# Kernel optimization log

Measured on AMD Instinct MI355X. Metric: run time of the kernel, lower is better.

The kernel has to match this reference:

```python
import jax, jax.numpy as jnp
import numpy as np

D = 512  # feature_dim


def setup_inputs() -> dict:
    key = jax.random.key(0)
    ks = jax.random.split(key, 10)
    s = 1.0 / np.sqrt(D)
    s2 = 1.0 / np.sqrt(2 * D)
    return {
        "X": jax.random.normal(ks[0], (8, 2048, D), dtype=jnp.float32),
        "Y": jax.random.normal(ks[1], (8, 2048, D), dtype=jnp.float32),
        "W_xq": jax.random.uniform(ks[2], (D, D), jnp.float32, -s, s),
        "b_xq": jax.random.uniform(ks[3], (D,), jnp.float32, -s, s),
        "W_yq": jax.random.uniform(ks[4], (D, D), jnp.float32, -s, s),
        "b_yq": jax.random.uniform(ks[5], (D,), jnp.float32, -s, s),
        "W_fk": jax.random.uniform(ks[6], (D, 2 * D), jnp.float32, -s2, s2),
        "b_fk": jax.random.uniform(ks[7], (D,), jnp.float32, -s2, s2),
        "W_fv": jax.random.uniform(ks[8], (D, 2 * D), jnp.float32, -s2, s2),
        "b_fv": jax.random.uniform(ks[9], (D,), jnp.float32, -s2, s2),
    }


def reference(X, Y, W_xq, b_xq, W_yq, b_yq, W_fk, b_fk, W_fv, b_fv):
    # Dropout is evaluated in eval mode (identity).
    scale = 1.0 / jnp.sqrt(jnp.asarray(D, X.dtype))
    Q1 = jnp.einsum('bsd,ed->bse', X, W_xq) + b_xq  # [B,S,D]
    Q2 = jnp.einsum('bsd,ed->bse', Y, W_yq) + b_yq
    Q_cat = jnp.concatenate([Q1, Q2], axis=-1)      # [B,S,2D]
    K_f = jnp.einsum('bsc,ec->bse', Q_cat, W_fk) + b_fk
    V_f = jnp.einsum('bsc,ec->bse', Q_cat, W_fv) + b_fv

    def attend(Q):
        scores = jnp.einsum('bqd,bkd->bqk', Q, K_f) * scale  # [B,S,S]
        A = jax.nn.softmax(scores, axis=-1)
        return jnp.einsum('bqk,bkd->bqd', A, V_f)

    U_A1 = X + attend(Q1)
    U_A2 = Y + attend(Q2)
    return U_A1 + U_A2
```

## Files before the change

### kernel.cpp

```cpp
#include <hip/hip_runtime.h>


#define B_    8
#define S_    2048
#define D_    512
#define M_TOT (B_ * S_)

typedef __bf16 bf16_t;
typedef __bf16 bf16x8 __attribute__((ext_vector_type(8)));
typedef __bf16 bf16x4 __attribute__((ext_vector_type(4)));
typedef float  f32x4  __attribute__((ext_vector_type(4)));

typedef __attribute__((address_space(1))) const void* gas_cv;
typedef __attribute__((address_space(3))) void*       las_v;

__device__ __forceinline__ f32x4 mfma16(bf16x8 a, bf16x8 b, f32x4 c) {
    return __builtin_amdgcn_mfma_f32_16x16x32_bf16(a, b, c, 0, 0, 0);
}
__device__ __forceinline__ void load_lds16(const void* g, void* l) {
    __builtin_amdgcn_global_load_lds((gas_cv)g, (las_v)l, 16, 0, 0);
}

__global__ __launch_bounds__(256) void k_qgemm(
    const float* __restrict__ X, const float* __restrict__ Y,
    const float* __restrict__ Wxq, const float* __restrict__ bxq,
    const float* __restrict__ Wyq, const float* __restrict__ byq,
    bf16_t* __restrict__ Qcat)
{
    __shared__ __attribute__((aligned(16))) bf16_t Al[128 * 40];
    __shared__ __attribute__((aligned(16))) bf16_t Bl[128 * 40];
    const int m0 = blockIdx.x * 128;
    const int n0 = blockIdx.y * 128;
    const bool second = (n0 >= 512);
    const float* A    = second ? Y : X;
    const float* W    = second ? Wyq : Wxq;
    const float* bias = second ? byq : bxq;
    const int nw = n0 & 511;
    const int t    = threadIdx.x;
    const int lane = t & 63;
    const int wv   = t >> 6;
    const int wm   = (wv & 1) * 64;
    const int wn   = (wv >> 1) * 64;
    const int l15  = lane & 15;
    const int quad = lane >> 4;

    f32x4 acc[4][4] = {};

    for (int k0 = 0; k0 < 512; k0 += 32) {
        __syncthreads();
#pragma unroll
        for (int p = 0; p < 4; ++p) {
            const int lin = p * 256 + t;
            const int row = lin >> 3;
            const int ch  = (lin & 7) * 4;
            const float4 va = *(const float4*)(A + (size_t)(m0 + row) * 512 + k0 + ch);
            bf16x4 pa = { (bf16_t)va.x, (bf16_t)va.y, (bf16_t)va.z, (bf16_t)va.w };
            *(bf16x4*)(Al + row * 40 + ch) = pa;
            const float4 vb = *(const float4*)(W + (size_t)(nw + row) * 512 + k0 + ch);
            bf16x4 pb = { (bf16_t)vb.x, (bf16_t)vb.y, (bf16_t)vb.z, (bf16_t)vb.w };
            *(bf16x4*)(Bl + row * 40 + ch) = pb;
        }
        __syncthreads();
        bf16x8 af[4], bfr[4];
#pragma unroll
        for (int i = 0; i < 4; ++i)
            af[i] = *(const bf16x8*)(Al + (wm + i * 16 + l15) * 40 + quad * 8);
#pragma unroll
        for (int i = 0; i < 4; ++i)
            bfr[i] = *(const bf16x8*)(Bl + (wn + i * 16 + l15) * 40 + quad * 8);
#pragma unroll
        for (int mt = 0; mt < 4; ++mt)
#pragma unroll
            for (int nt = 0; nt < 4; ++nt)
                acc[mt][nt] = mfma16(af[mt], bfr[nt], acc[mt][nt]);
    }

#pragma unroll
    for (int nt = 0; nt < 4; ++nt) {
        const int col  = n0 + wn + nt * 16 + l15;
        const float bv = bias[col & 511];
#pragma unroll
        for (int mt = 0; mt < 4; ++mt) {
            const int rowb = m0 + wm + mt * 16 + quad * 4;
#pragma unroll
            for (int r = 0; r < 4; ++r)
                Qcat[(size_t)(rowb + r) * 1024 + col] = (bf16_t)(acc[mt][nt][r] + bv);
        }
    }
}

__global__ __launch_bounds__(256) void k_kvgemm(
    const bf16_t* __restrict__ Qcat,
    const float* __restrict__ Wfk, const float* __restrict__ bfk,
    const float* __restrict__ Wfv, const float* __restrict__ bfv,
    bf16_t* __restrict__ Kf, bf16_t* __restrict__ Vt)
{
    __shared__ __attribute__((aligned(16))) union {
        struct { bf16_t Al[128 * 40]; bf16_t Bl[128 * 40]; } g;
        bf16_t T[128 * 132];
    } sm;
    const int m0 = blockIdx.x * 128;
    const int n0 = blockIdx.y * 128;
    const bool isV = (n0 >= 512);
    const float* W    = isV ? Wfv : Wfk;
    const float* bias = isV ? bfv : bfk;
    const int nw = n0 & 511;
    const int t    = threadIdx.x;
    const int lane = t & 63;
    const int wv   = t >> 6;
    const int wm   = (wv & 1) * 64;
    const int wn   = (wv >> 1) * 64;
    const int l15  = lane & 15;
    const int quad = lane >> 4;

    f32x4 acc[4][4] = {};

    for (int k0 = 0; k0 < 1024; k0 += 32) {
        __syncthreads();
#pragma unroll
        for (int p = 0; p < 2; ++p) {
            const int lin = p * 256 + t;
            const int row = lin >> 2;
            const int ch  = (lin & 3) * 8;
            *(bf16x8*)(sm.g.Al + row * 40 + ch) =
                *(const bf16x8*)(Qcat + (size_t)(m0 + row) * 1024 + k0 + ch);
        }
#pragma unroll
        for (int p = 0; p < 4; ++p) {
            const int lin = p * 256 + t;
            const int row = lin >> 3;
            const int ch  = (lin & 7) * 4;
            const float4 vb = *(const float4*)(W + (size_t)(nw + row) * 1024 + k0 + ch);
            bf16x4 pb = { (bf16_t)vb.x, (bf16_t)vb.y, (bf16_t)vb.z, (bf16_t)vb.w };
            *(bf16x4*)(sm.g.Bl + row * 40 + ch) = pb;
        }
        __syncthreads();
        bf16x8 af[4], bfr[4];
#pragma unroll
        for (int i = 0; i < 4; ++i)
            af[i] = *(const bf16x8*)(sm.g.Al + (wm + i * 16 + l15) * 40 + quad * 8);
#pragma unroll
        for (int i = 0; i < 4; ++i)
            bfr[i] = *(const bf16x8*)(sm.g.Bl + (wn + i * 16 + l15) * 40 + quad * 8);
#pragma unroll
        for (int mt = 0; mt < 4; ++mt)
#pragma unroll
            for (int nt = 0; nt < 4; ++nt)
                acc[mt][nt] = mfma16(af[mt], bfr[nt], acc[mt][nt]);
    }

    if (!isV) {
#pragma unroll
        for (int nt = 0; nt < 4; ++nt) {
            const int col  = n0 + wn + nt * 16 + l15;
            const float bv = bias[col];
#pragma unroll
            for (int mt = 0; mt < 4; ++mt) {
                const int rowb = m0 + wm + mt * 16 + quad * 4;
#pragma unroll
                for (int r = 0; r < 4; ++r)
                    Kf[(size_t)(rowb + r) * 512 + col] = (bf16_t)(acc[mt][nt][r] + bv);
            }
        }
    } else {
        __syncthreads();
#pragma unroll
        for (int nt = 0; nt < 4; ++nt) {
            const int dl = wn + nt * 16 + l15;
            const float bv = bias[nw + dl];
#pragma unroll
            for (int mt = 0; mt < 4; ++mt) {
                const int sl = wm + mt * 16 + quad * 4;
#pragma unroll
                for (int r = 0; r < 4; ++r)
                    sm.T[dl * 132 + sl + r] = (bf16_t)(acc[mt][nt][r] + bv);
            }
        }
        __syncthreads();
        const int bb = m0 >> 11;
        const int sb = m0 & 2047;
        const int half = lane >> 5;
        const int sl4  = (lane & 31) * 4;
#pragma unroll
        for (int i = 0; i < 16; ++i) {
            const int dl = wv * 32 + i * 2 + half;
            const bf16x4 v = *(const bf16x4*)(sm.T + dl * 132 + sl4);
            *(bf16x4*)(Vt + (size_t)(bb * 512 + nw + dl) * 2048 + sb + sl4) = v;
        }
    }
}

__global__ __launch_bounds__(256, 2) void k_attn(
    const bf16_t* __restrict__ Qcat, const bf16_t* __restrict__ Kf,
    const bf16_t* __restrict__ Vt,
    const float* __restrict__ X, const float* __restrict__ Y,
    float* __restrict__ out, bf16_t* __restrict__ attn,
    const int mode, const int which)
{
    __shared__ __attribute__((aligned(16))) bf16_t Kl[2][32 * 520];
    __shared__ __attribute__((aligned(16))) bf16_t Pl[2][64 * 40];
    __shared__ float lsumL[64];

    const int b = blockIdx.y;
    const int w = (mode == 0) ? (int)blockIdx.z : which;
    const int t    = threadIdx.x;
    const int lane = t & 63;
    const int wv   = t >> 6;
    const int l15  = lane & 15;
    const int quad = lane >> 4;
    const int q0   = blockIdx.x * 64;
    const int qw   = q0 + wv * 16;

    const bf16_t* Kbase = Kf + (size_t)b * S_ * 512;
    const bf16_t* Vbase = Vt + ((size_t)b * 512 + wv * 128) * S_;

    bf16x8 aq[16];
    {
        const bf16_t* qp = Qcat + (size_t)(b * S_ + qw + l15) * 1024 + w * 512 + quad * 8;
#pragma unroll
        for (int ks = 0; ks < 16; ++ks) aq[ks] = *(const bf16x8*)(qp + ks * 32);
    }

    f32x4 acc[4][8] = {};
    float lacc[4] = { 0.f, 0.f, 0.f, 0.f };
    const float sc2 = 0.04419417382415922f * 1.4426950408889634f;

#pragma unroll
    for (int p = 0; p < 8; ++p) {
        const int row = wv * 8 + p;
        load_lds16(Kbase + (size_t)row * 512 + lane * 8, Kl[0] + row * 520);
    }
    __syncthreads();

    {
#pragma unroll
        for (int p = 0; p < 8; ++p) {
            const int row = wv * 8 + p;
            load_lds16(Kbase + (size_t)(32 + row) * 512 + lane * 8, Kl[1] + row * 520);
        }
        f32x4 s0a = {}, s0b = {}, s1a = {}, s1b = {};
#pragma unroll
        for (int ks = 0; ks < 16; ks += 2) {
            const bf16x8 b0 = *(const bf16x8*)(Kl[0] + l15 * 520 + ks * 32 + quad * 8);
            const bf16x8 b1 = *(const bf16x8*)(Kl[0] + (16 + l15) * 520 + ks * 32 + quad * 8);
            const bf16x8 c0 = *(const bf16x8*)(Kl[0] + l15 * 520 + (ks + 1) * 32 + quad * 8);
            const bf16x8 c1 = *(const bf16x8*)(Kl[0] + (16 + l15) * 520 + (ks + 1) * 32 + quad * 8);
            s0a = mfma16(aq[ks], b0, s0a);
            s1a = mfma16(aq[ks], b1, s1a);
            s0b = mfma16(aq[ks + 1], c0, s0b);
            s1b = mfma16(aq[ks + 1], c1, s1b);
        }
        const f32x4 sA = s0a + s0b, sB = s1a + s1b;
#pragma unroll
        for (int r = 0; r < 4; ++r) {
            const float p0 = exp2f(sA[r] * sc2);
            const float p1 = exp2f(sB[r] * sc2);
            lacc[r] += p0 + p1;
            Pl[0][(wv * 16 + quad * 4 + r) * 40 + l15] = (bf16_t)p0;
            Pl[0][(wv * 16 + quad * 4 + r) * 40 + 16 + l15] = (bf16_t)p1;
        }
        __syncthreads();
    }

    for (int kb = 1; kb < 64; ++kb) {
        const int cur = kb & 1;
        const int prv = cur ^ 1;

        {
            const bf16_t* src = Kbase + (size_t)(kb + 1) * 32 * 512;
#pragma unroll
            for (int p = 0; p < 8; ++p) {
                const int row = wv * 8 + p;
                load_lds16(src + (size_t)row * 512 + lane * 8, Kl[prv] + row * 520);
            }
        }

        bf16x8 vb[8];
#pragma unroll
        for (int i = 0; i < 8; ++i)
            vb[i] = *(const bf16x8*)(Vbase + (size_t)(i * 16 + l15) * S_ +
                                     (kb - 1) * 32 + quad * 8);

        f32x4 s0a = {}, s0b = {}, s1a = {}, s1b = {};
#pragma unroll
        for (int ks = 0; ks < 16; ks += 2) {
            const bf16x8 b0 = *(const bf16x8*)(Kl[cur] + l15 * 520 + ks * 32 + quad * 8);
            const bf16x8 b1 = *(const bf16x8*)(Kl[cur] + (16 + l15) * 520 + ks * 32 + quad * 8);
            const bf16x8 c0 = *(const bf16x8*)(Kl[cur] + l15 * 520 + (ks + 1) * 32 + quad * 8);
            const bf16x8 c1 = *(const bf16x8*)(Kl[cur] + (16 + l15) * 520 + (ks + 1) * 32 + quad * 8);
            s0a = mfma16(aq[ks], b0, s0a);
            s1a = mfma16(aq[ks], b1, s1a);
            s0b = mfma16(aq[ks + 1], c0, s0b);
            s1b = mfma16(aq[ks + 1], c1, s1b);
        }

        {
            bf16x8 ap[4];
#pragma unroll
            for (int qt = 0; qt < 4; ++qt)
                ap[qt] = *(const bf16x8*)(Pl[prv] + (qt * 16 + l15) * 40 + quad * 8);
#pragma unroll
            for (int dt = 0; dt < 8; ++dt)
#pragma unroll
                for (int qt = 0; qt < 4; ++qt)
                    acc[qt][dt] = mfma16(ap[qt], vb[dt], acc[qt][dt]);
        }

        const f32x4 sA = s0a + s0b, sB = s1a + s1b;
#pragma unroll
        for (int r = 0; r < 4; ++r) {
            const float p0 = exp2f(sA[r] * sc2);
            const float p1 = exp2f(sB[r] * sc2);
            lacc[r] += p0 + p1;
            Pl[cur][(wv * 16 + quad * 4 + r) * 40 + l15] = (bf16_t)p0;
            Pl[cur][(wv * 16 + quad * 4 + r) * 40 + 16 + l15] = (bf16_t)p1;
        }

        __syncthreads();
    }

    {
        bf16x8 vb[8];
#pragma unroll
        for (int i = 0; i < 8; ++i)
            vb[i] = *(const bf16x8*)(Vbase + (size_t)(i * 16 + l15) * S_ +
                                     63 * 32 + quad * 8);
        bf16x8 ap[4];
#pragma unroll
        for (int qt = 0; qt < 4; ++qt)
            ap[qt] = *(const bf16x8*)(Pl[1] + (qt * 16 + l15) * 40 + quad * 8);
#pragma unroll
        for (int dt = 0; dt < 8; ++dt)
#pragma unroll
            for (int qt = 0; qt < 4; ++qt)
                acc[qt][dt] = mfma16(ap[qt], vb[dt], acc[qt][dt]);
    }

    {
        float lrow[4];
#pragma unroll
        for (int r = 0; r < 4; ++r) {
            float v = lacc[r];
#pragma unroll
            for (int off = 1; off < 16; off <<= 1) v += __shfl_xor(v, off, 64);
            lrow[r] = v;
        }
        if (l15 == 0) {
#pragma unroll
            for (int r = 0; r < 4; ++r) lsumL[wv * 16 + quad * 4 + r] = lrow[r];
        }
    }
    __syncthreads();

#pragma unroll
    for (int qt = 0; qt < 4; ++qt) {
        f32x4 inv;
#pragma unroll
        for (int r = 0; r < 4; ++r) inv[r] = 1.0f / lsumL[qt * 16 + quad * 4 + r];
#pragma unroll
        for (int dt = 0; dt < 8; ++dt) {
            const int d = wv * 128 + dt * 16 + l15;
#pragma unroll
            for (int r = 0; r < 4; ++r) {
                const float v = acc[qt][dt][r] * inv[r];
                const size_t idx =
                    (size_t)(b * S_ + q0 + qt * 16 + quad * 4 + r) * 512 + d;
                if (mode == 0)      attn[(size_t)w * M_TOT * 512 + idx] = (bf16_t)v;
                else if (mode == 1) out[idx] = X[idx] + Y[idx] + v;
                else                out[idx] += v;
            }
        }
    }
}

__global__ __launch_bounds__(256) void k_add(
    const float* __restrict__ X, const float* __restrict__ Y,
    const bf16_t* __restrict__ a0, const bf16_t* __restrict__ a1,
    float* __restrict__ out)
{
    const size_t i = ((size_t)blockIdx.x * 256 + threadIdx.x) * 4;
    const float4 x = *(const float4*)(X + i);
    const float4 y = *(const float4*)(Y + i);
    const bf16x4 v0 = *(const bf16x4*)(a0 + i);
    const bf16x4 v1 = *(const bf16x4*)(a1 + i);
    float4 o;
    o.x = x.x + y.x + (float)v0[0] + (float)v1[0];
    o.y = x.y + y.y + (float)v0[1] + (float)v1[1];
    o.z = x.z + y.z + (float)v0[2] + (float)v1[2];
    o.w = x.w + y.w + (float)v0[3] + (float)v1[3];
    *(float4*)(out + i) = o;
}

extern "C" void kernel_launch(void* const* d_in, const int* in_sizes, int n_in,
                              void* d_out, int out_size, void* d_ws, size_t ws_size,
                              hipStream_t stream)
{
    const float* X   = (const float*)d_in[0];
    const float* Y   = (const float*)d_in[1];
    const float* Wxq = (const float*)d_in[2];
    const float* bxq = (const float*)d_in[3];
    const float* Wyq = (const float*)d_in[4];
    const float* byq = (const float*)d_in[5];
    const float* Wfk = (const float*)d_in[6];
    const float* bfk = (const float*)d_in[7];
    const float* Wfv = (const float*)d_in[8];
    const float* bfv = (const float*)d_in[9];
    float* out = (float*)d_out;
    char*  ws  = (char*)d_ws;

    bf16_t* Qcat = (bf16_t*)(ws);
    bf16_t* Kf   = (bf16_t*)(ws + (size_t)33554432);
    bf16_t* Vt   = (bf16_t*)(ws + (size_t)50331648);
    bf16_t* attn = (bf16_t*)(ws + (size_t)67108864);
    const bool big = ws_size >= (size_t)100663296;

    k_qgemm<<<dim3(128, 8), 256, 0, stream>>>(X, Y, Wxq, bxq, Wyq, byq, Qcat);
    k_kvgemm<<<dim3(128, 8), 256, 0, stream>>>(Qcat, Wfk, bfk, Wfv, bfv, Kf, Vt);
    if (big) {
        k_attn<<<dim3(32, 8, 2), 256, 0, stream>>>(Qcat, Kf, Vt, X, Y, out, attn, 0, 0);
        k_add<<<dim3(8192), 256, 0, stream>>>(X, Y, attn, attn + (size_t)M_TOT * 512, out);
    } else {
        k_attn<<<dim3(32, 8, 1), 256, 0, stream>>>(Qcat, Kf, Vt, X, Y, out, attn, 1, 0);
        k_attn<<<dim3(32, 8, 1), 256, 0, stream>>>(Qcat, Kf, Vt, X, Y, out, attn, 2, 1);
    }
}
```

Baseline: 474.6 us.

## Pre-convert X/Y to bf16, use direct-to-LDS loads in GEMMs, tweak attention scheduling

Adds a conversion kernel that writes bf16 copies of X and Y, so a new Q-projection GEMM and the KV GEMM can stream A tiles with global_load_lds straight into unpadded LDS. The attention kernel shrinks the P-tile row pitch to 36 and splits its LDS reads into two 4-wide halves, hoists the V loads ahead of the K prefetch, and raises wave priority with s_setprio around the MFMA sections. The aim is to cut register staging and global-load latency in the GEMMs and to overlap memory with compute in attention. The cost is an extra pass over X and Y plus possible LDS bank conflicts, since the A tiles are no longer padded.

```diff
diff --git a/kernel.cpp b/kernel.cpp
--- a/kernel.cpp
+++ b/kernel.cpp
@@ -19,6 +19,21 @@
 }
 __device__ __forceinline__ void load_lds16(const void* g, void* l) {
     __builtin_amdgcn_global_load_lds((gas_cv)g, (las_v)l, 16, 0, 0);
+}
+
+__global__ __launch_bounds__(256) void k_cvt(
+    const float* __restrict__ X, const float* __restrict__ Y,
+    bf16_t* __restrict__ Xb, bf16_t* __restrict__ Yb)
+{
+    const int n4 = M_TOT * 512 / 4;
+    for (int i = blockIdx.x * 256 + threadIdx.x; i < n4; i += 2048 * 256) {
+        const float4 x = *(const float4*)(X + (size_t)i * 4);
+        bf16x4 px = { (bf16_t)x.x, (bf16_t)x.y, (bf16_t)x.z, (bf16_t)x.w };
+        *(bf16x4*)(Xb + (size_t)i * 4) = px;
+        const float4 y = *(const float4*)(Y + (size_t)i * 4);
+        bf16x4 py = { (bf16_t)y.x, (bf16_t)y.y, (bf16_t)y.z, (bf16_t)y.w };
+        *(bf16x4*)(Yb + (size_t)i * 4) = py;
+    }
 }
 
 __global__ __launch_bounds__(256) void k_qgemm(
@@ -89,6 +104,76 @@
     }
 }
 
+__global__ __launch_bounds__(256) void k_qgemm_dma(
+    const bf16_t* __restrict__ Xb, const bf16_t* __restrict__ Yb,
+    const float* __restrict__ Wxq, const float* __restrict__ bxq,
+    const float* __restrict__ Wyq, const float* __restrict__ byq,
+    bf16_t* __restrict__ Qcat)
+{
+    __shared__ __attribute__((aligned(16))) bf16_t Al[128 * 32];
+    __shared__ __attribute__((aligned(16))) bf16_t Bl[128 * 32];
+    const int m0 = blockIdx.x * 128;
+    const int n0 = blockIdx.y * 128;
+    const bool second = (n0 >= 512);
+    const bf16_t* A   = second ? Yb : Xb;
+    const float* W    = second ? Wyq : Wxq;
+    const float* bias = second ? byq : bxq;
+    const int nw = n0 & 511;
+    const int t    = threadIdx.x;
+    const int lane = t & 63;
+    const int wv   = t >> 6;
+    const int wm   = (wv & 1) * 64;
+    const int wn   = (wv >> 1) * 64;
+    const int l15  = lane & 15;
+    const int quad = lane >> 4;
+
+    const int ar0 = t >> 2,          ac0 = (t & 3) * 8;
+    const int ar1 = (256 + t) >> 2,  ac1 = ((256 + t) & 3) * 8;
+
+    f32x4 acc[4][4] = {};
+
+    for (int k0 = 0; k0 < 512; k0 += 32) {
+        __syncthreads();
+        load_lds16(A + (size_t)(m0 + ar0) * 512 + k0 + ac0, Al + t * 8);
+        load_lds16(A + (size_t)(m0 + ar1) * 512 + k0 + ac1, Al + (256 + t) * 8);
+#pragma unroll
+        for (int p = 0; p < 4; ++p) {
+            const int lin = p * 256 + t;
+            const int row = lin >> 3;
+            const int ch  = (lin & 7) * 4;
+            const float4 vb = *(const float4*)(W + (size_t)(nw + row) * 512 + k0 + ch);
+            bf16x4 pb = { (bf16_t)vb.x, (bf16_t)vb.y, (bf16_t)vb.z, (bf16_t)vb.w };
+            *(bf16x4*)(Bl + row * 32 + ch) = pb;
+        }
+        __syncthreads();
+        bf16x8 af[4], bfr[4];
+#pragma unroll
+        for (int i = 0; i < 4; ++i)
+            af[i] = *(const bf16x8*)(Al + (wm + i * 16 + l15) * 32 + quad * 8);
+#pragma unroll
+        for (int i = 0; i < 4; ++i)
+            bfr[i] = *(const bf16x8*)(Bl + (wn + i * 16 + l15) * 32 + quad * 8);
+#pragma unroll
+        for (int mt = 0; mt < 4; ++mt)
+#pragma unroll
+            for (int nt = 0; nt < 4; ++nt)
+                acc[mt][nt] = mfma16(af[mt], bfr[nt], acc[mt][nt]);
+    }
+
+#pragma unroll
+    for (int nt = 0; nt < 4; ++nt) {
+        const int col  = n0 + wn + nt * 16 + l15;
+        const float bv = bias[col & 511];
+#pragma unroll
+        for (int mt = 0; mt < 4; ++mt) {
+            const int rowb = m0 + wm + mt * 16 + quad * 4;
+#pragma unroll
+            for (int r = 0; r < 4; ++r)
+                Qcat[(size_t)(rowb + r) * 1024 + col] = (bf16_t)(acc[mt][nt][r] + bv);
+        }
+    }
+}
+
 __global__ __launch_bounds__(256) void k_kvgemm(
     const bf16_t* __restrict__ Qcat,
     const float* __restrict__ Wfk, const float* __restrict__ bfk,
@@ -96,7 +181,7 @@
     bf16_t* __restrict__ Kf, bf16_t* __restrict__ Vt)
 {
     __shared__ __attribute__((aligned(16))) union {
-        struct { bf16_t Al[128 * 40]; bf16_t Bl[128 * 40]; } g;
+        struct { bf16_t Al[128 * 32]; bf16_t Bl[128 * 32]; } g;
         bf16_t T[128 * 132];
     } sm;
     const int m0 = blockIdx.x * 128;
@@ -113,18 +198,15 @@
     const int l15  = lane & 15;
     const int quad = lane >> 4;
 
+    const int ar0 = t >> 2,          ac0 = (t & 3) * 8;
+    const int ar1 = (256 + t) >> 2,  ac1 = ((256 + t) & 3) * 8;
+
     f32x4 acc[4][4] = {};
 
     for (int k0 = 0; k0 < 1024; k0 += 32) {
         __syncthreads();
-#pragma unroll
-        for (int p = 0; p < 2; ++p) {
-            const int lin = p * 256 + t;
-            const int row = lin >> 2;
-            const int ch  = (lin & 3) * 8;
-            *(bf16x8*)(sm.g.Al + row * 40 + ch) =
-                *(const bf16x8*)(Qcat + (size_t)(m0 + row) * 1024 + k0 + ch);
-        }
+        load_lds16(Qcat + (size_t)(m0 + ar0) * 1024 + k0 + ac0, sm.g.Al + t * 8);
+        load_lds16(Qcat + (size_t)(m0 + ar1) * 1024 + k0 + ac1, sm.g.Al + (256 + t) * 8);
 #pragma unroll
         for (int p = 0; p < 4; ++p) {
             const int lin = p * 256 + t;
@@ -132,16 +214,16 @@
             const int ch  = (lin & 7) * 4;
             const float4 vb = *(const float4*)(W + (size_t)(nw + row) * 1024 + k0 + ch);
             bf16x4 pb = { (bf16_t)vb.x, (bf16_t)vb.y, (bf16_t)vb.z, (bf16_t)vb.w };
-            *(bf16x4*)(sm.g.Bl + row * 40 + ch) = pb;
+            *(bf16x4*)(sm.g.Bl + row * 32 + ch) = pb;
         }
         __syncthreads();
         bf16x8 af[4], bfr[4];
 #pragma unroll
         for (int i = 0; i < 4; ++i)
-            af[i] = *(const bf16x8*)(sm.g.Al + (wm + i * 16 + l15) * 40 + quad * 8);
+            af[i] = *(const bf16x8*)(sm.g.Al + (wm + i * 16 + l15) * 32 + quad * 8);
 #pragma unroll
         for (int i = 0; i < 4; ++i)
-            bfr[i] = *(const bf16x8*)(sm.g.Bl + (wn + i * 16 + l15) * 40 + quad * 8);
+            bfr[i] = *(const bf16x8*)(sm.g.Bl + (wn + i * 16 + l15) * 32 + quad * 8);
 #pragma unroll
         for (int mt = 0; mt < 4; ++mt)
 #pragma unroll
@@ -198,7 +280,7 @@
     const int mode, const int which)
 {
     __shared__ __attribute__((aligned(16))) bf16_t Kl[2][32 * 520];
-    __shared__ __attribute__((aligned(16))) bf16_t Pl[2][64 * 40];
+    __shared__ __attribute__((aligned(16))) bf16_t Pl[2][64 * 36];
     __shared__ float lsumL[64];
 
     const int b = blockIdx.y;
@@ -239,6 +321,7 @@
             load_lds16(Kbase + (size_t)(32 + row) * 512 + lane * 8, Kl[1] + row * 520);
         }
         f32x4 s0a = {}, s0b = {}, s1a = {}, s1b = {};
+        __builtin_amdgcn_s_setprio(1);
 #pragma unroll
         for (int ks = 0; ks < 16; ks += 2) {
             const bf16x8 b0 = *(const bf16x8*)(Kl[0] + l15 * 520 + ks * 32 + quad * 8);
@@ -250,14 +333,15 @@
             s0b = mfma16(aq[ks + 1], c0, s0b);
             s1b = mfma16(aq[ks + 1], c1, s1b);
         }
+        __builtin_amdgcn_s_setprio(0);
         const f32x4 sA = s0a + s0b, sB = s1a + s1b;
 #pragma unroll
         for (int r = 0; r < 4; ++r) {
             const float p0 = exp2f(sA[r] * sc2);
             const float p1 = exp2f(sB[r] * sc2);
             lacc[r] += p0 + p1;
-            Pl[0][(wv * 16 + quad * 4 + r) * 40 + l15] = (bf16_t)p0;
-            Pl[0][(wv * 16 + quad * 4 + r) * 40 + 16 + l15] = (bf16_t)p1;
+            Pl[0][(wv * 16 + quad * 4 + r) * 36 + l15] = (bf16_t)p0;
+            Pl[0][(wv * 16 + quad * 4 + r) * 36 + 16 + l15] = (bf16_t)p1;
         }
         __syncthreads();
     }
@@ -265,6 +349,12 @@
     for (int kb = 1; kb < 64; ++kb) {
         const int cur = kb & 1;
         const int prv = cur ^ 1;
+
+        bf16x8 vb[8];
+#pragma unroll
+        for (int i = 0; i < 8; ++i)
+            vb[i] = *(const bf16x8*)(Vbase + (size_t)(i * 16 + l15) * S_ +
+                                     (kb - 1) * 32 + quad * 8);
 
         {
             const bf16_t* src = Kbase + (size_t)(kb + 1) * 32 * 512;
@@ -275,12 +365,7 @@
             }
         }
 
-        bf16x8 vb[8];
-#pragma unroll
-        for (int i = 0; i < 8; ++i)
-            vb[i] = *(const bf16x8*)(Vbase + (size_t)(i * 16 + l15) * S_ +
-                                     (kb - 1) * 32 + quad * 8);
-
+        __builtin_amdgcn_s_setprio(1);
         f32x4 s0a = {}, s0b = {}, s1a = {}, s1b = {};
 #pragma unroll
         for (int ks = 0; ks < 16; ks += 2) {
@@ -297,14 +382,18 @@
         {
             bf16x8 ap[4];
 #pragma unroll
-            for (int qt = 0; qt < 4; ++qt)
-                ap[qt] = *(const bf16x8*)(Pl[prv] + (qt * 16 + l15) * 40 + quad * 8);
+            for (int qt = 0; qt < 4; ++qt) {
+                const bf16x4 lo = *(const bf16x4*)(Pl[prv] + (qt * 16 + l15) * 36 + quad * 8);
+                const bf16x4 hi = *(const bf16x4*)(Pl[prv] + (qt * 16 + l15) * 36 + quad * 8 + 4);
+                ap[qt] = __builtin_shufflevector(lo, hi, 0, 1, 2, 3, 4, 5, 6, 7);
+            }
 #pragma unroll
             for (int dt = 0; dt < 8; ++dt)
 #pragma unroll
                 for (int qt = 0; qt < 4; ++qt)
                     acc[qt][dt] = mfma16(ap[qt], vb[dt], acc[qt][dt]);
         }
+        __builtin_amdgcn_s_setprio(0);
 
         const f32x4 sA = s0a + s0b, sB = s1a + s1b;
 #pragma unroll
@@ -312,8 +401,8 @@
             const float p0 = exp2f(sA[r] * sc2);
             const float p1 = exp2f(sB[r] * sc2);
             lacc[r] += p0 + p1;
-            Pl[cur][(wv * 16 + quad * 4 + r) * 40 + l15] = (bf16_t)p0;
-            Pl[cur][(wv * 16 + quad * 4 + r) * 40 + 16 + l15] = (bf16_t)p1;
+            Pl[cur][(wv * 16 + quad * 4 + r) * 36 + l15] = (bf16_t)p0;
+            Pl[cur][(wv * 16 + quad * 4 + r) * 36 + 16 + l15] = (bf16_t)p1;
         }
 
         __syncthreads();
@@ -327,8 +416,11 @@
                                      63 * 32 + quad * 8);
         bf16x8 ap[4];
 #pragma unroll
-        for (int qt = 0; qt < 4; ++qt)
-            ap[qt] = *(const bf16x8*)(Pl[1] + (qt * 16 + l15) * 40 + quad * 8);
+        for (int qt = 0; qt < 4; ++qt) {
+            const bf16x4 lo = *(const bf16x4*)(Pl[1] + (qt * 16 + l15) * 36 + quad * 8);
+            const bf16x4 hi = *(const bf16x4*)(Pl[1] + (qt * 16 + l15) * 36 + quad * 8 + 4);
+            ap[qt] = __builtin_shufflevector(lo, hi, 0, 1, 2, 3, 4, 5, 6, 7);
+        }
 #pragma unroll
         for (int dt = 0; dt < 8; ++dt)
 #pragma unroll
@@ -412,9 +504,16 @@
     bf16_t* Kf   = (bf16_t*)(ws + (size_t)33554432);
     bf16_t* Vt   = (bf16_t*)(ws + (size_t)50331648);
     bf16_t* attn = (bf16_t*)(ws + (size_t)67108864);
+    bf16_t* Xb   = (bf16_t*)(ws + (size_t)67108864);
+    bf16_t* Yb   = (bf16_t*)(ws + (size_t)83886080);
     const bool big = ws_size >= (size_t)100663296;
 
-    k_qgemm<<<dim3(128, 8), 256, 0, stream>>>(X, Y, Wxq, bxq, Wyq, byq, Qcat);
+    if (big) {
+        k_cvt<<<dim3(2048), 256, 0, stream>>>(X, Y, Xb, Yb);
+        k_qgemm_dma<<<dim3(128, 8), 256, 0, stream>>>(Xb, Yb, Wxq, bxq, Wyq, byq, Qcat);
+    } else {
+        k_qgemm<<<dim3(128, 8), 256, 0, stream>>>(X, Y, Wxq, bxq, Wyq, byq, Qcat);
+    }
     k_kvgemm<<<dim3(128, 8), 256, 0, stream>>>(Qcat, Wfk, bfk, Wfv, bfv, Kf, Vt);
     if (big) {
         k_attn<<<dim3(32, 8, 2), 256, 0, stream>>>(Qcat, Kf, Vt, X, Y, out, attn, 0, 0);
```

After: 529.1 us. 1.11x slower.
